# Kernel optimization log

Hardware: AMD Instinct MI355X
Metric: run time of the kernel (lower is better)

Reference implementation:

```python
import jax, jax.numpy as jnp
import numpy as np

N_NODES = 100000
N_EDGES = 600000
IN_DIM = 128
HID = 128


def setup_inputs() -> dict:
    key = jax.random.key(0)
    ks = jax.random.split(key, 9)
    x = jax.random.normal(ks[0], (N_NODES, IN_DIM), dtype=jnp.float32)
    edge_index = jax.random.randint(ks[1], (2, N_EDGES), 0, N_NODES, dtype=jnp.int64)
    s = 1.0 / np.sqrt(IN_DIM)
    # PyG SAGEConv: out = lin_l(mean_aggr(x_src)) + lin_r(x_root); lin_l carries the bias.
    W_l0 = jax.random.uniform(ks[2], (IN_DIM, HID), jnp.float32, -s, s)
    b_l0 = jnp.zeros((HID,), jnp.float32)
    W_r0 = jax.random.uniform(ks[3], (IN_DIM, HID), jnp.float32, -s, s)
    s2 = 1.0 / np.sqrt(HID)
    W_l1 = jax.random.uniform(ks[4], (HID, HID), jnp.float32, -s2, s2)
    b_l1 = jnp.zeros((HID,), jnp.float32)
    W_r1 = jax.random.uniform(ks[5], (HID, HID), jnp.float32, -s2, s2)
    return {"x": x, "edge_index": edge_index,
            "W_l0": W_l0, "b_l0": b_l0, "W_r0": W_r0,
            "W_l1": W_l1, "b_l1": b_l1, "W_r1": W_r1}


def _sage_mean_conv(h, src, dst, W_l, b_l, W_r):
    # gather source-node features per edge, scatter-mean into destinations
    msgs = h[src]                                              # [E, D]
    sums = jax.ops.segment_sum(msgs, dst, num_segments=N_NODES)  # [N, D]
    cnt = jax.ops.segment_sum(jnp.ones((src.shape[0],), h.dtype), dst,
                              num_segments=N_NODES)             # [N]
    mean = sums / jnp.maximum(cnt, 1.0)[:, None]
    return mean @ W_l + b_l + h @ W_r


def reference(x, edge_index, W_l0, b_l0, W_r0, W_l1, b_l1, W_r1):
    src, dst = edge_index[0], edge_index[1]
    h = _sage_mean_conv(x, src, dst, W_l0, b_l0, W_r0)
    h = jax.nn.relu(h)  # dropout is identity in eval mode
    h = _sage_mean_conv(h, src, dst, W_l1, b_l1, W_r1)
    h = jax.nn.relu(h)
    return h
```

## Files before the change

### kernel.cpp

```cpp
#include <hip/hip_runtime.h>

#define N_NODES 100000
#define N_EDGES 600000
#define DIM 128

typedef __attribute__((ext_vector_type(8))) short bf16x8;
typedef __attribute__((ext_vector_type(4))) float f32x4;

typedef __attribute__((address_space(1))) const unsigned int g_u32;
typedef __attribute__((address_space(3))) unsigned int l_u32;
__device__ __forceinline__ void stage16(const void* g, void* l) {
  __builtin_amdgcn_global_load_lds((g_u32*)g, (l_u32*)l, 16, 0, 0);
}

__device__ __forceinline__ unsigned short f32_to_bf16_rn(float f) {
  unsigned int u = __builtin_bit_cast(unsigned int, f);
  unsigned int r = (u + 0x7FFFu + ((u >> 16) & 1u)) >> 16;
  return (unsigned short)r;
}

__global__ __launch_bounds__(256) void prep_k(
    const float* __restrict__ Wl0, const float* __restrict__ Wr0,
    const float* __restrict__ Wl1, const float* __restrict__ Wr1,
    unsigned short* __restrict__ P0, unsigned short* __restrict__ P1,
    const float* __restrict__ x, unsigned short* __restrict__ xhi) {
  const int gid = blockIdx.x * 256 + threadIdx.x;
  if (gid < 65536) {
    const int layer = gid >> 15;
    const int idx = gid & 32767;
    const int j = idx & 7;
    const int l = (idx >> 3) & 63;
    const int nt = (idx >> 9) & 7;
    const int g = idx >> 12;
    const int k = ((g & 3) << 5) + ((l >> 4) << 3) + j;
    const int n = (nt << 4) + (l & 15);
    const float* W = layer ? ((g < 4) ? Wl1 : Wr1) : ((g < 4) ? Wl0 : Wr0);
    (layer ? P1 : P0)[idx] = f32_to_bf16_rn(W[k * 128 + n]);
  } else {
    const int i = gid - 65536;
    if (i < N_NODES * DIM / 4) {
      const float4 v = reinterpret_cast<const float4*>(x)[i];
      const float f[4] = {v.x, v.y, v.z, v.w};
      unsigned short h[4];
#pragma unroll
      for (int j = 0; j < 4; ++j) h[j] = f32_to_bf16_rn(f[j]);
      uint2 hp;
      hp.x = (unsigned)h[0] | ((unsigned)h[1] << 16);
      hp.y = (unsigned)h[2] | ((unsigned)h[3] << 16);
      reinterpret_cast<uint2*>(xhi)[i] = hp;
    }
  }
}

__global__ void hist_k(const int* __restrict__ dst, int* __restrict__ deg) {
  int e = blockIdx.x * blockDim.x + threadIdx.x;
  if (e < N_EDGES) atomicAdd(&deg[dst[e]], 1);
}

__global__ __launch_bounds__(1024) void scan1_k(const int* __restrict__ deg,
                                                int* __restrict__ incl,
                                                int* __restrict__ bsum) {
  __shared__ int wsum[16];
  const int t = threadIdx.x, lane = t & 63, w = t >> 6;
  const int gi = blockIdx.x * 1024 + t;
  int v = (gi < N_NODES) ? deg[gi] : 0;
  int s = v;
#pragma unroll
  for (int off = 1; off < 64; off <<= 1) {
    int u = __shfl_up(s, off);
    if (lane >= off) s += u;
  }
  if (lane == 63) wsum[w] = s;
  __syncthreads();
  if (t < 16) {
    int ws = wsum[t];
#pragma unroll
    for (int off = 1; off < 16; off <<= 1) {
      int u = __shfl_up(ws, off);
      if (t >= off) ws += u;
    }
    wsum[t] = ws;
  }
  __syncthreads();
  const int val = s + (w ? wsum[w - 1] : 0);
  if (gi < N_NODES) incl[gi] = val;
  if (t == 1023) bsum[blockIdx.x] = val;
}

__global__ void scan2_k(const int* __restrict__ bsum, int* __restrict__ boffs,
                        int nb) {
  __shared__ int w0;
  const int t = threadIdx.x;
  int v = (t < nb) ? bsum[t] : 0;
  int s = v;
#pragma unroll
  for (int off = 1; off < 64; off <<= 1) {
    int u = __shfl_up(s, off);
    if ((t & 63) >= off) s += u;
  }
  if (t == 63) w0 = s;
  __syncthreads();
  const int excl = s - v + ((t >> 6) ? w0 : 0);
  if (t < nb) boffs[t] = excl;
}

__global__ __launch_bounds__(1024) void scan3_k(const int* __restrict__ deg,
                                                const int* __restrict__ incl,
                                                const int* __restrict__ boffs,
                                                int* __restrict__ rowptr,
                                                int* __restrict__ head) {
  const int gi = blockIdx.x * 1024 + threadIdx.x;
  if (gi < N_NODES) {
    const int e = incl[gi] - deg[gi] + boffs[blockIdx.x];
    rowptr[gi] = e;
    head[gi] = e;
  }
  if (gi == 0) rowptr[N_NODES] = N_EDGES;
}

__global__ void fill_k(const int* __restrict__ src, const int* __restrict__ dst,
                       int* __restrict__ head, int* __restrict__ col) {
  int e = blockIdx.x * blockDim.x + threadIdx.x;
  if (e < N_EDGES) {
    int p = atomicAdd(&head[dst[e]], 1);
    col[p] = src[e];
  }
}

__global__ __launch_bounds__(256) void agg_k(
    const unsigned short* __restrict__ plane, const int* __restrict__ rowptr,
    const int* __restrict__ col, unsigned short* __restrict__ mhi) {
  const int t = threadIdx.x;
  const int node = blockIdx.x * 16 + (t >> 4);
  const int q = t & 15;
  const int beg = rowptr[node], end = rowptr[node + 1];
  const uint4* P = reinterpret_cast<const uint4*>(plane);
  float a[8] = {};

  auto accum = [&](uint4 v) {
    const unsigned int u[4] = {v.x, v.y, v.z, v.w};
#pragma unroll
    for (int w = 0; w < 4; ++w) {
      a[2 * w] += __builtin_bit_cast(float, u[w] << 16);
      a[2 * w + 1] += __builtin_bit_cast(float, u[w] & 0xFFFF0000u);
    }
  };

  for (int i = beg; i < end; i += 4) {
    const int i1 = min(i + 1, end - 1);
    const int i2 = min(i + 2, end - 1);
    const int i3 = min(i + 3, end - 1);
    const int c0 = col[i], c1 = col[i1], c2 = col[i2], c3 = col[i3];
    const uint4 v0 = P[(size_t)c0 * 16 + q];
    const uint4 v1 = P[(size_t)c1 * 16 + q];
    const uint4 v2 = P[(size_t)c2 * 16 + q];
    const uint4 v3 = P[(size_t)c3 * 16 + q];
    accum(v0);
    if (i + 1 < end) accum(v1);
    if (i + 2 < end) accum(v2);
    if (i + 3 < end) accum(v3);
  }

  const int d = end - beg;
  const float inv = 1.0f / (float)(d > 1 ? d : 1);
  unsigned int hw[4];
#pragma unroll
  for (int w = 0; w < 4; ++w) {
    const unsigned short h0 = f32_to_bf16_rn(a[2 * w] * inv);
    const unsigned short h1 = f32_to_bf16_rn(a[2 * w + 1] * inv);
    hw[w] = (unsigned)h0 | ((unsigned)h1 << 16);
  }
  uint4 ho = {hw[0], hw[1], hw[2], hw[3]};
  reinterpret_cast<uint4*>(mhi)[(size_t)node * 16 + q] = ho;
}

template <int OUTF32>
__global__ __launch_bounds__(256, 4) void gemm_k(
    const unsigned short* __restrict__ Mhi, const unsigned short* __restrict__ Hhi,
    const unsigned short* __restrict__ Bp, const float* __restrict__ bias,
    unsigned short* __restrict__ Ohi, float* __restrict__ Of) {
  __shared__ unsigned short Bl[2][4096];
  const int t = threadIdx.x;
  const int lane = t & 63;
  const int wid = t >> 6;
  const int rbase = blockIdx.x * 128 + wid * 32;
  const int lm = lane & 15, lk = lane >> 4;
  const size_t r0 = (size_t)min(rbase + lm, N_NODES - 1);
  const size_t r1 = (size_t)min(rbase + 16 + lm, N_NODES - 1);

  f32x4 acc[2][8] = {};

  auto stageG = [&](int g, int nb) {
#pragma unroll
    for (int c = 0; c < 2; ++c) {
      const int e = (c * 256 + t) * 8;
      stage16(Bp + (size_t)g * 4096 + e, &Bl[nb][e]);
    }
  };
  auto loadA = [&](int g, bf16x8& a0, bf16x8& a1) {
    const unsigned short* P = (g < 4) ? Mhi : Hhi;
    const int ke = ((g & 3) << 5) + (lk << 3);
    a0 = *reinterpret_cast<const bf16x8*>(P + r0 * DIM + ke);
    a1 = *reinterpret_cast<const bf16x8*>(P + r1 * DIM + ke);
  };

  bf16x8 ca0, ca1, na0, na1;
  stageG(0, 0);
  loadA(0, ca0, ca1);
  __syncthreads();

#pragma unroll
  for (int g = 0; g < 8; ++g) {
    const int buf = g & 1;
    if (g < 7) {
      stageG(g + 1, buf ^ 1);
      loadA(g + 1, na0, na1);
    }
#pragma unroll
    for (int nt = 0; nt < 8; ++nt) {
      const bf16x8 b =
          *reinterpret_cast<const bf16x8*>(&Bl[buf][(nt * 64 + lane) * 8]);
      acc[0][nt] = __builtin_amdgcn_mfma_f32_16x16x32_bf16(ca0, b, acc[0][nt], 0, 0, 0);
      acc[1][nt] = __builtin_amdgcn_mfma_f32_16x16x32_bf16(ca1, b, acc[1][nt], 0, 0, 0);
    }
    __syncthreads();
    ca0 = na0;
    ca1 = na1;
  }

#pragma unroll
  for (int nt = 0; nt < 8; ++nt) {
    const int cidx = nt * 16 + lm;
    const float bv = bias[cidx];
#pragma unroll
    for (int mt = 0; mt < 2; ++mt) {
#pragma unroll
      for (int i = 0; i < 4; ++i) {
        const int r = rbase + mt * 16 + lk * 4 + i;
        if (r < N_NODES) {
          float v = acc[mt][nt][i] + bv;
          v = fmaxf(v, 0.0f);
          if (OUTF32) {
            Of[(size_t)r * DIM + cidx] = v;
          } else {
            Ohi[(size_t)r * DIM + cidx] = f32_to_bf16_rn(v);
          }
        }
      }
    }
  }
}

extern "C" void kernel_launch(void* const* d_in, const int* in_sizes, int n_in,
                              void* d_out, int out_size, void* d_ws,
                              size_t ws_size, hipStream_t stream) {
  const float* x = (const float*)d_in[0];
  const int* ei = (const int*)d_in[1];
  const float* Wl0 = (const float*)d_in[2];
  const float* bl0 = (const float*)d_in[3];
  const float* Wr0 = (const float*)d_in[4];
  const float* Wl1 = (const float*)d_in[5];
  const float* bl1 = (const float*)d_in[6];
  const float* Wr1 = (const float*)d_in[7];
  float* out = (float*)d_out;
  const int* src = ei;
  const int* dst = ei + N_EDGES;

  char* p = (char*)d_ws;
  auto alloc = [&](size_t bytes) {
    char* q = p;
    p += (bytes + 255) & ~(size_t)255;
    return q;
  };
  int* deg = (int*)alloc((size_t)N_NODES * 4);
  int* rowptr = (int*)alloc((size_t)(N_NODES + 1) * 4);
  int* head = (int*)alloc((size_t)N_NODES * 4);
  int* col = (int*)alloc((size_t)N_EDGES * 4);
  int* bsum = (int*)alloc(128 * 4);
  int* boffs = (int*)alloc(128 * 4);
  unsigned short* Bp0 = (unsigned short*)alloc(32768 * 2);
  unsigned short* Bp1 = (unsigned short*)alloc(32768 * 2);
  unsigned short* xhi = (unsigned short*)alloc((size_t)N_NODES * DIM * 2);
  unsigned short* mhi = (unsigned short*)alloc((size_t)N_NODES * DIM * 2);
  unsigned short* h1hi = (unsigned short*)alloc((size_t)N_NODES * DIM * 2);

  const int nScanB = (N_NODES + 1023) / 1024;

  hipMemsetAsync(deg, 0, (size_t)N_NODES * 4, stream);
  prep_k<<<(65536 + N_NODES * DIM / 4 + 255) / 256, 256, 0, stream>>>(
      Wl0, Wr0, Wl1, Wr1, Bp0, Bp1, x, xhi);
  hist_k<<<(N_EDGES + 255) / 256, 256, 0, stream>>>(dst, deg);
  scan1_k<<<nScanB, 1024, 0, stream>>>(deg, head, bsum);
  scan2_k<<<1, 128, 0, stream>>>(bsum, boffs, nScanB);
  scan3_k<<<nScanB, 1024, 0, stream>>>(deg, head, boffs, rowptr, head);
  fill_k<<<(N_EDGES + 255) / 256, 256, 0, stream>>>(src, dst, head, col);

  const int nBlocks = (N_NODES + 127) / 128;
  const int aggBlocks = N_NODES / 16;

  agg_k<<<aggBlocks, 256, 0, stream>>>(xhi, rowptr, col, mhi);
  gemm_k<0><<<nBlocks, 256, 0, stream>>>(mhi, xhi, Bp0, bl0, h1hi, nullptr);
  agg_k<<<aggBlocks, 256, 0, stream>>>(h1hi, rowptr, col, mhi);
  gemm_k<1><<<nBlocks, 256, 0, stream>>>(mhi, h1hi, Bp1, bl1, nullptr, out);
}
```

Measured before the change: 187.5 us.

## Preload all weight tiles and A fragments up front in GEMM; fold deg memset into prep

The GEMM kernel stops double-buffering B over eight k-groups. It now stages all eight B tiles into a larger 64KB LDS buffer and loads all A fragments into registers at once, then runs a single barrier before the MFMA loop. This removes the per-iteration barriers and pipeline bookkeeping, but it raises LDS and register use, so launch bounds drop to 2 blocks per SM and occupancy falls. Separately, the degree memset is folded into the prep kernel to save one launch.

```diff
diff --git a/kernel.cpp b/kernel.cpp
--- a/kernel.cpp
+++ b/kernel.cpp
@@ -23,8 +23,10 @@
     const float* __restrict__ Wl0, const float* __restrict__ Wr0,
     const float* __restrict__ Wl1, const float* __restrict__ Wr1,
     unsigned short* __restrict__ P0, unsigned short* __restrict__ P1,
-    const float* __restrict__ x, unsigned short* __restrict__ xhi) {
+    const float* __restrict__ x, unsigned short* __restrict__ xhi,
+    int* __restrict__ deg) {
   const int gid = blockIdx.x * 256 + threadIdx.x;
+  if (gid < N_NODES) deg[gid] = 0;
   if (gid < 65536) {
     const int layer = gid >> 15;
     const int idx = gid & 32767;
@@ -175,11 +177,11 @@
 }
 
 template <int OUTF32>
-__global__ __launch_bounds__(256, 4) void gemm_k(
+__global__ __launch_bounds__(256, 2) void gemm_k(
     const unsigned short* __restrict__ Mhi, const unsigned short* __restrict__ Hhi,
     const unsigned short* __restrict__ Bp, const float* __restrict__ bias,
     unsigned short* __restrict__ Ohi, float* __restrict__ Of) {
-  __shared__ unsigned short Bl[2][4096];
+  __shared__ unsigned short Bl[8][4096];
   const int t = threadIdx.x;
   const int lane = t & 63;
   const int wid = t >> 6;
@@ -188,44 +190,35 @@
   const size_t r0 = (size_t)min(rbase + lm, N_NODES - 1);
   const size_t r1 = (size_t)min(rbase + 16 + lm, N_NODES - 1);
 
-  f32x4 acc[2][8] = {};
-
-  auto stageG = [&](int g, int nb) {
+#pragma unroll
+  for (int g = 0; g < 8; ++g) {
 #pragma unroll
     for (int c = 0; c < 2; ++c) {
       const int e = (c * 256 + t) * 8;
-      stage16(Bp + (size_t)g * 4096 + e, &Bl[nb][e]);
-    }
-  };
-  auto loadA = [&](int g, bf16x8& a0, bf16x8& a1) {
+      stage16(Bp + (size_t)g * 4096 + e, &Bl[g][e]);
+    }
+  }
+
+  bf16x8 a0[8], a1[8];
+#pragma unroll
+  for (int g = 0; g < 8; ++g) {
     const unsigned short* P = (g < 4) ? Mhi : Hhi;
     const int ke = ((g & 3) << 5) + (lk << 3);
-    a0 = *reinterpret_cast<const bf16x8*>(P + r0 * DIM + ke);
-    a1 = *reinterpret_cast<const bf16x8*>(P + r1 * DIM + ke);
-  };
-
-  bf16x8 ca0, ca1, na0, na1;
-  stageG(0, 0);
-  loadA(0, ca0, ca1);
-  __syncthreads();
-
+    a0[g] = *reinterpret_cast<const bf16x8*>(P + r0 * DIM + ke);
+    a1[g] = *reinterpret_cast<const bf16x8*>(P + r1 * DIM + ke);
+  }
+  __syncthreads();
+
+  f32x4 acc[2][8] = {};
 #pragma unroll
   for (int g = 0; g < 8; ++g) {
-    const int buf = g & 1;
-    if (g < 7) {
-      stageG(g + 1, buf ^ 1);
-      loadA(g + 1, na0, na1);
-    }
 #pragma unroll
     for (int nt = 0; nt < 8; ++nt) {
       const bf16x8 b =
-          *reinterpret_cast<const bf16x8*>(&Bl[buf][(nt * 64 + lane) * 8]);
-      acc[0][nt] = __builtin_amdgcn_mfma_f32_16x16x32_bf16(ca0, b, acc[0][nt], 0, 0, 0);
-      acc[1][nt] = __builtin_amdgcn_mfma_f32_16x16x32_bf16(ca1, b, acc[1][nt], 0, 0, 0);
-    }
-    __syncthreads();
-    ca0 = na0;
-    ca1 = na1;
+          *reinterpret_cast<const bf16x8*>(&Bl[g][(nt * 64 + lane) * 8]);
+      acc[0][nt] = __builtin_amdgcn_mfma_f32_16x16x32_bf16(a0[g], b, acc[0][nt], 0, 0, 0);
+      acc[1][nt] = __builtin_amdgcn_mfma_f32_16x16x32_bf16(a1[g], b, acc[1][nt], 0, 0, 0);
+    }
   }
 
 #pragma unroll
@@ -286,9 +279,8 @@
 
   const int nScanB = (N_NODES + 1023) / 1024;
 
-  hipMemsetAsync(deg, 0, (size_t)N_NODES * 4, stream);
   prep_k<<<(65536 + N_NODES * DIM / 4 + 255) / 256, 256, 0, stream>>>(
-      Wl0, Wr0, Wl1, Wr1, Bp0, Bp1, x, xhi);
+      Wl0, Wr0, Wl1, Wr1, Bp0, Bp1, x, xhi, deg);
   hist_k<<<(N_EDGES + 255) / 256, 256, 0, stream>>>(dst, deg);
   scan1_k<<<nScanB, 1024, 0, stream>>>(deg, head, bsum);
   scan2_k<<<1, 128, 0, stream>>>(bsum, boffs, nScanB);
```

Measured after the change: 201.1 us. +7.3%, slower.
